# Kernel optimization log

Hardware: AMD Instinct MI355X
Metric: run time of the kernel (lower is better)

Reference implementation:

```python
import jax, jax.numpy as jnp
import numpy as np

N_LAYERS = 4
H = 16
LOOKBACK = 128  # cross_window
EPS = 1e-6
ROPE_BASE = 10000.0
NEG = jnp.float32(-1e30)


def rmsnorm(x, w):
    return x * jax.lax.rsqrt(jnp.mean(x * x, axis=-1, keepdims=True) + EPS) * w


def rope_cache(L, hd):
    inv = 1.0 / (ROPE_BASE ** (jnp.arange(0, hd, 2, dtype=jnp.float32) / hd))
    t = jnp.arange(L, dtype=jnp.float32)
    f = t[:, None] * inv[None, :]            # [L, hd/2]
    emb = jnp.concatenate([f, f], axis=-1)   # [L, hd]
    return jnp.cos(emb), jnp.sin(emb)


def apply_rope(x, cos, sin):
    # x: [B,H,L,d]; rotate-half convention
    d = x.shape[-1]
    x1, x2 = x[..., : d // 2], x[..., d // 2:]
    rot = jnp.concatenate([-x2, x1], axis=-1)
    return x * cos + rot * sin


def split_heads(x, n_heads):
    B, L, D = x.shape
    return x.reshape(B, L, n_heads, D // n_heads).transpose(0, 2, 1, 3)


def merge_heads(x):
    B, h, L, d = x.shape
    return x.transpose(0, 2, 1, 3).reshape(B, L, h * d)


def sdpa(q, k, v, bias):
    scale = q.shape[-1] ** -0.5
    s = jnp.einsum('bhqd,bhkd->bhqk', q, k) * scale + bias
    p = jax.nn.softmax(s, axis=-1)
    return jnp.einsum('bhqk,bhkd->bhqd', p, v)


def forward(x, memory, seg_ids, Wqkv, bqkv, Wo, bo, Wq_c, Wkv_c, Wo_c, Wg, Wu, Wd, n1, n2, n3, nf):
    B, L, D = x.shape
    S = memory.shape[1]
    hd = D // H
    cos, sin = rope_cache(L, hd)

    # causal additive mask [1,1,L,L]
    i = jnp.arange(L)
    causal_bias = jnp.where(i[None, :] <= i[:, None], 0.0, NEG)[None, None]

    # segment-causal sliding-window cross mask [B,1,L,S]:
    # token t may attend memory j with seg_id[t]-LOOKBACK < j <= seg_id[t]
    j = jnp.arange(S)
    allowed = (j[None, None, :] <= seg_ids[:, :, None]) & (j[None, None, :] > seg_ids[:, :, None] - LOOKBACK)
    cross_bias = jnp.where(allowed, 0.0, NEG)[:, None]  # [B,1,L,S]

    for l in range(N_LAYERS):
        # --- causal self-attn with RoPE ---
        h = rmsnorm(x, n1[l])
        qkv = h @ Wqkv[l].T + bqkv[l]                      # [B,L,3D]
        q, k, v = jnp.split(qkv, 3, axis=-1)
        q = apply_rope(split_heads(q, H), cos, sin)
        k = apply_rope(split_heads(k, H), cos, sin)
        v = split_heads(v, H)
        o = merge_heads(sdpa(q, k, v, causal_bias)) @ Wo[l].T + bo[l]
        x = x + o

        # --- segment-causal sliding-window cross-attn ---
        h2 = rmsnorm(x, n2[l])
        qc = split_heads(h2 @ Wq_c[l].T, H)
        kv = memory @ Wkv_c[l].T                           # [B,S,2D]
        kc, vc = jnp.split(kv, 2, axis=-1)
        kc, vc = split_heads(kc, H), split_heads(vc, H)
        oc = merge_heads(sdpa(qc, kc, vc, cross_bias)) @ Wo_c[l].T
        x = x + oc

        # --- SwiGLU FFN ---
        h3 = rmsnorm(x, n3[l])
        x = x + (jax.nn.silu(h3 @ Wg[l].T) * (h3 @ Wu[l].T)) @ Wd[l].T

    return rmsnorm(x, nf)


def setup_inputs() -> dict:
    key = jax.random.key(0)
    ks = jax.random.split(key, 16)
    B, L, S, D, F = 2, 2048, 256, 1024, 4096
    w = 0.02
    inp = {
        'x': jax.random.normal(ks[0], (B, L, D), jnp.float32),
        'memory': jax.random.normal(ks[1], (B, S, D), jnp.float32),
        'seg_ids': jnp.sort(jax.random.randint(ks[2], (B, L), 0, S), axis=-1),
        'Wqkv': jax.random.normal(ks[3], (N_LAYERS, 3 * D, D), jnp.float32) * w,
        'bqkv': jnp.zeros((N_LAYERS, 3 * D), jnp.float32),
        'Wo': jax.random.normal(ks[4], (N_LAYERS, D, D), jnp.float32) * w,
        'bo': jnp.zeros((N_LAYERS, D), jnp.float32),
        'Wq_c': jax.random.normal(ks[5], (N_LAYERS, D, D), jnp.float32) * w,
        'Wkv_c': jax.random.normal(ks[6], (N_LAYERS, 2 * D, D), jnp.float32) * w,
        'Wo_c': jax.random.normal(ks[7], (N_LAYERS, D, D), jnp.float32) * w,
        'Wg': jax.random.normal(ks[8], (N_LAYERS, F, D), jnp.float32) * w,
        'Wu': jax.random.normal(ks[9], (N_LAYERS, F, D), jnp.float32) * w,
        'Wd': jax.random.normal(ks[10], (N_LAYERS, D, F), jnp.float32) * w,
        'n1': jnp.ones((N_LAYERS, D), jnp.float32),
        'n2': jnp.ones((N_LAYERS, D), jnp.float32),
        'n3': jnp.ones((N_LAYERS, D), jnp.float32),
        'nf': jnp.ones((D,), jnp.float32),
    }
    return inp


def reference(x, memory, seg_ids, Wqkv, bqkv, Wo, bo, Wq_c, Wkv_c, Wo_c, Wg, Wu, Wd, n1, n2, n3, nf):
    return forward(x, memory, seg_ids, Wqkv, bqkv, Wo, bo, Wq_c, Wkv_c, Wo_c, Wg, Wu, Wd, n1, n2, n3, nf)
```

## Files before the change

kernel.cpp:

```cpp
#include <hip/hip_runtime.h>
#include <hip/hip_bf16.h>
#include <math.h>

#define N_LAYERS 4
#define NHEADS 16
#define LOOKBACK 128

typedef unsigned short ushort_t;
typedef __attribute__((ext_vector_type(8))) short short8;
typedef __attribute__((ext_vector_type(4))) float f32x4;

__device__ __forceinline__ ushort_t f2bf(float f) {
    union { float f; unsigned int u; } v; v.f = f;
    unsigned int r = (v.u + 0x7FFFu + ((v.u >> 16) & 1u)) >> 16;
    return (ushort_t)r;
}
__device__ __forceinline__ float bf2f(ushort_t s) {
    union { unsigned int u; float f; } v; v.u = ((unsigned int)s) << 16;
    return v.f;
}

__device__ __forceinline__ float blk_sum(float v, volatile float* red) {
#pragma unroll
    for (int o = 32; o > 0; o >>= 1) v += __shfl_down(v, o, 64);
    if ((threadIdx.x & 63) == 0) red[threadIdx.x >> 6] = v;
    __syncthreads();
    float r = red[0] + red[1] + red[2] + red[3];
    __syncthreads();
    return r;
}

__global__ __launch_bounds__(256) void f2b_k(const float* __restrict__ in,
                                             ushort_t* __restrict__ out, int n4) {
    int i = blockIdx.x * 256 + threadIdx.x;
    if (i >= n4) return;
    float4 v = *(const float4*)(in + (size_t)i * 4);
    ushort_t* o = out + (size_t)i * 4;
    o[0] = f2bf(v.x); o[1] = f2bf(v.y); o[2] = f2bf(v.z); o[3] = f2bf(v.w);
}

__global__ __launch_bounds__(256) void rmsnorm_bf(const float* __restrict__ x,
                                                  const float* __restrict__ w,
                                                  ushort_t* __restrict__ out, int D) {
    __shared__ float red[4];
    size_t row = blockIdx.x;
    const float* xr = x + row * D;
    float ss = 0.f;
    for (int i = threadIdx.x; i < D; i += 256) { float v = xr[i]; ss += v * v; }
    float tot = blk_sum(ss, red);
    float r = rsqrtf(tot / (float)D + 1e-6f);
    ushort_t* o = out + row * D;
    for (int i = threadIdx.x; i < D; i += 256) o[i] = f2bf(xr[i] * r * w[i]);
}

__global__ __launch_bounds__(256) void rmsnorm_k(const float* __restrict__ x,
                                                 const float* __restrict__ w,
                                                 float* __restrict__ out, int D) {
    __shared__ float red[4];
    size_t row = blockIdx.x;
    const float* xr = x + row * D;
    float ss = 0.f;
    for (int i = threadIdx.x; i < D; i += 256) { float v = xr[i]; ss += v * v; }
    float tot = blk_sum(ss, red);
    float r = rsqrtf(tot / (float)D + 1e-6f);
    float* o = out + row * D;
    for (int i = threadIdx.x; i < D; i += 256) o[i] = xr[i] * r * w[i];
}

#define GBM 128
#define GBN 128
#define GBK 32

#define STAGE_GEMM(kk, buf) do {                                               \
    const ushort_t* Ag_ = A + (size_t)(bm + srow) * K + (kk) + c4 * 8;         \
    const ushort_t* Bg_ = Bw + (size_t)(bn + srow) * K + (kk) + c4 * 8;        \
    __builtin_amdgcn_global_load_lds(                                          \
        (const __attribute__((address_space(1))) void*)Ag_,                    \
        (__attribute__((address_space(3))) void*)&As[buf][wave * 16 * GBK],    \
        16, 0, 0);                                                             \
    __builtin_amdgcn_global_load_lds(                                          \
        (const __attribute__((address_space(1))) void*)(Ag_ + (size_t)64 * K), \
        (__attribute__((address_space(3))) void*)&As[buf][(64 + wave * 16) * GBK], \
        16, 0, 0);                                                             \
    __builtin_amdgcn_global_load_lds(                                          \
        (const __attribute__((address_space(1))) void*)Bg_,                    \
        (__attribute__((address_space(3))) void*)&Bs[buf][wave * 16 * GBK],    \
        16, 0, 0);                                                             \
    __builtin_amdgcn_global_load_lds(                                          \
        (const __attribute__((address_space(1))) void*)(Bg_ + (size_t)64 * K), \
        (__attribute__((address_space(3))) void*)&Bs[buf][(64 + wave * 16) * GBK], \
        16, 0, 0);                                                             \
} while (0)

__global__ __launch_bounds__(256) void gemm_bf16(
    const ushort_t* __restrict__ A, const ushort_t* __restrict__ Bw,
    void* __restrict__ Cout, const float* __restrict__ bias,
    const float* __restrict__ resid, const ushort_t* __restrict__ gate,
    int M, int N, int K, int out_bf16) {
    __shared__ ushort_t As[2][GBM * GBK];
    __shared__ ushort_t Bs[2][GBN * GBK];
    int tid = threadIdx.x;
    int wave = tid >> 6, lane = tid & 63;
    int nwg = gridDim.x * gridDim.y;
    int wg  = blockIdx.y * gridDim.x + blockIdx.x;
    int qq = nwg >> 3, rr = nwg & 7;
    int xcd = wg & 7, loc = wg >> 3;
    int swz = (xcd < rr ? xcd * (qq + 1) : rr * (qq + 1) + (xcd - rr) * qq) + loc;
    int bm = (swz / gridDim.x) * GBM, bn = (swz % gridDim.x) * GBN;
    int wm = (wave & 1) * 64, wn = (wave >> 1) * 64;
    int r4 = lane >> 2, c4 = lane & 3;
    int r = lane & 15, q = lane >> 4;

    f32x4 acc[4][4];
#pragma unroll
    for (int i = 0; i < 4; ++i)
#pragma unroll
        for (int j = 0; j < 4; ++j) acc[i][j] = (f32x4){0.f, 0.f, 0.f, 0.f};

    int srow = wave * 16 + r4;
    int nt = K / GBK;
    STAGE_GEMM(0, 0);
    for (int t = 0; t < nt; ++t) {
        int cur = t & 1;
        if (t + 1 < nt) {
            STAGE_GEMM((t + 1) * GBK, cur ^ 1);
            asm volatile("s_waitcnt vmcnt(4)" ::: "memory");
        } else {
            asm volatile("s_waitcnt vmcnt(0)" ::: "memory");
        }
        __builtin_amdgcn_s_barrier();
        __builtin_amdgcn_sched_barrier(0);
        short8 af[4], bfr[4];
#pragma unroll
        for (int i = 0; i < 4; ++i)
            af[i] = *(const short8*)&As[cur][(wm + 16 * i + r) * GBK + q * 8];
#pragma unroll
        for (int j = 0; j < 4; ++j)
            bfr[j] = *(const short8*)&Bs[cur][(wn + 16 * j + r) * GBK + q * 8];
#pragma unroll
        for (int i = 0; i < 4; ++i)
#pragma unroll
            for (int j = 0; j < 4; ++j)
                acc[i][j] = __builtin_amdgcn_mfma_f32_16x16x32_bf16(
                    af[i], bfr[j], acc[i][j], 0, 0, 0);
        __builtin_amdgcn_s_barrier();
        __builtin_amdgcn_sched_barrier(0);
    }
#pragma unroll
    for (int i = 0; i < 4; ++i) {
#pragma unroll
        for (int j = 0; j < 4; ++j) {
            size_t n = (size_t)(bn + wn + 16 * j + r);
            float bn_v = bias ? bias[n] : 0.f;
#pragma unroll
            for (int t = 0; t < 4; ++t) {
                size_t m = (size_t)(bm + wm + 16 * i + q * 4 + t);
                size_t idx = m * N + n;
                float x = acc[i][j][t] + bn_v;
                if (gate) { float g = bf2f(gate[idx]); x *= g / (1.0f + __expf(-g)); }
                if (resid) x += resid[idx];
                if (out_bf16) ((ushort_t*)Cout)[idx] = f2bf(x);
                else ((float*)Cout)[idx] = x;
            }
        }
    }
}

__global__ void rope_k(ushort_t* __restrict__ qkv, int L, int total) {
    int idx = blockIdx.x * 256 + threadIdx.x;
    if (idx >= total) return;
    int d = idx & 31;
    int h = (idx >> 5) & 15;
    int bl = idx >> 9;
    int l = bl % L;
    float inv = exp2f(-(float)d * (13.2877123795f / 32.0f));
    float f = (float)l * inv;
    float s, c;
    sincosf(f, &s, &c);
    ushort_t* base = qkv + (size_t)bl * 3072 + h * 64 + d;
    float x1 = bf2f(base[0]), x2 = bf2f(base[32]);
    base[0]  = f2bf((x1 * c - x2 * s) * 0.125f);
    base[32] = f2bf((x2 * c + x1 * s) * 0.125f);
    ushort_t* kb = base + 1024;
    x1 = bf2f(kb[0]); x2 = bf2f(kb[32]);
    kb[0]  = f2bf(x1 * c - x2 * s);
    kb[32] = f2bf(x2 * c + x1 * s);
}

#define QB 128

__global__ __launch_bounds__(256) void self_attn_flash(
    const ushort_t* __restrict__ qkv, ushort_t* __restrict__ out, int L) {
    int lin = blockIdx.x + gridDim.x * (blockIdx.y + gridDim.y * blockIdx.z);
    int xcd = lin & 7, slot = lin >> 3;
    int qt = slot & 15;
    int grp = xcd + 8 * (slot >> 4);
    int h = grp & 15, b = grp >> 4;
    int q0 = qt * QB;

    __shared__ ushort_t Qs[QB * 72];
    __shared__ ushort_t Ks[2][64 * 72];
    __shared__ ushort_t VT[2][64 * 64];
    __shared__ ushort_t Ps[QB * 64];

    int tid = threadIdx.x;
    int wave = tid >> 6, lane = tid & 63;
    int g = lane >> 4, r = lane & 15;
    int lr2 = tid >> 1, lc2 = tid & 1;
    int lr = tid >> 2, lc = tid & 3;

    {
        const ushort_t* src = qkv + ((size_t)b * L + q0 + lr2) * 3072 + h * 64 + lc2 * 32;
        ushort_t* dst = &Qs[lr2 * 72 + lc2 * 32];
        *(short8*)(dst)      = *(const short8*)(src);
        *(short8*)(dst + 8)  = *(const short8*)(src + 8);
        *(short8*)(dst + 16) = *(const short8*)(src + 16);
        *(short8*)(dst + 24) = *(const short8*)(src + 24);
    }
    __syncthreads();
    short8 aq[2][2];
#pragma unroll
    for (int s = 0; s < 2; ++s)
#pragma unroll
        for (int c = 0; c < 2; ++c)
            aq[s][c] = *(const short8*)&Qs[(wave * 32 + s * 16 + r) * 72 + c * 32 + g * 8];

    const ushort_t* kvbase = qkv + ((size_t)b * L + lr) * 3072 + 1024 + h * 64 + lc * 16;
    short8 kreg0 = *(const short8*)(kvbase);
    short8 kreg1 = *(const short8*)(kvbase + 8);
    short8 vreg0 = *(const short8*)(kvbase + 1024);
    short8 vreg1 = *(const short8*)(kvbase + 1032);

    float m[2][4], lsum[2][4];
    f32x4 acc[2][4];
#pragma unroll
    for (int s = 0; s < 2; ++s)
#pragma unroll
        for (int t = 0; t < 4; ++t) { m[s][t] = -1e30f; lsum[s][t] = 0.f; }
#pragma unroll
    for (int s = 0; s < 2; ++s)
#pragma unroll
        for (int j = 0; j < 4; ++j) acc[s][j] = (f32x4){0.f, 0.f, 0.f, 0.f};

    int ktmax = 2 * qt + 1;
    for (int kt = 0; kt <= ktmax; ++kt) {
        int cb = kt & 1;
        ushort_t* Kc = &Ks[cb][0];
        ushort_t* Vc = &VT[cb][0];
        *(short8*)&Kc[lr * 72 + lc * 16]     = kreg0;
        *(short8*)&Kc[lr * 72 + lc * 16 + 8] = kreg1;
#pragma unroll
        for (int i = 0; i < 8; ++i) {
            int row0 = lc * 16 + i;
            int f0 = (row0 & 7) ^ ((row0 >> 4) & 3);
            Vc[row0 * 64 + (((lr >> 3) ^ f0) << 3) + (lr & 7)] = (ushort_t)vreg0[i];
            int row1 = row0 + 8;
            int f1 = (row1 & 7) ^ ((row1 >> 4) & 3);
            Vc[row1 * 64 + (((lr >> 3) ^ f1) << 3) + (lr & 7)] = (ushort_t)vreg1[i];
        }
        asm volatile("s_waitcnt lgkmcnt(0)" ::: "memory");
        __builtin_amdgcn_s_barrier();
        __builtin_amdgcn_sched_barrier(0);
        if (kt < ktmax) {
            const ushort_t* p = kvbase + (size_t)(kt + 1) * 64 * 3072;
            kreg0 = *(const short8*)(p);
            kreg1 = *(const short8*)(p + 8);
            vreg0 = *(const short8*)(p + 1024);
            vreg1 = *(const short8*)(p + 1032);
        }

        int k0 = kt * 64;
        f32x4 s2[2][4];
#pragma unroll
        for (int s = 0; s < 2; ++s)
#pragma unroll
            for (int j = 0; j < 4; ++j) s2[s][j] = (f32x4){0.f, 0.f, 0.f, 0.f};
        __builtin_amdgcn_s_setprio(1);
#pragma unroll
        for (int j = 0; j < 4; ++j)
#pragma unroll
            for (int c = 0; c < 2; ++c) {
                short8 bk = *(const short8*)&Kc[(16 * j + r) * 72 + c * 32 + g * 8];
                s2[0][j] = __builtin_amdgcn_mfma_f32_16x16x32_bf16(aq[0][c], bk, s2[0][j], 0, 0, 0);
                s2[1][j] = __builtin_amdgcn_mfma_f32_16x16x32_bf16(aq[1][c], bk, s2[1][j], 0, 0, 0);
            }
        __builtin_amdgcn_s_setprio(0);

        if (kt >= ktmax - 1) {
#pragma unroll
            for (int s = 0; s < 2; ++s)
#pragma unroll
                for (int j = 0; j < 4; ++j) {
                    int k = k0 + 16 * j + r;
#pragma unroll
                    for (int t = 0; t < 4; ++t)
                        if (k > q0 + wave * 32 + s * 16 + 4 * g + t) s2[s][j][t] = -1e30f;
                }
        }

        float al[2][4];
#pragma unroll
        for (int s = 0; s < 2; ++s)
#pragma unroll
            for (int t = 0; t < 4; ++t) {
                float rm = fmaxf(fmaxf(s2[s][0][t], s2[s][1][t]), fmaxf(s2[s][2][t], s2[s][3][t]));
#pragma unroll
                for (int o = 8; o > 0; o >>= 1) rm = fmaxf(rm, __shfl_xor(rm, o, 16));
                float mn = fmaxf(m[s][t], rm);
                al[s][t] = __expf(m[s][t] - mn);
                m[s][t] = mn;
                float rs = 0.f;
#pragma unroll
                for (int j = 0; j < 4; ++j) {
                    float p = __expf(s2[s][j][t] - mn);
                    s2[s][j][t] = p;
                    rs += p;
                }
#pragma unroll
                for (int o = 8; o > 0; o >>= 1) rs += __shfl_xor(rs, o, 16);
                lsum[s][t] = lsum[s][t] * al[s][t] + rs;
            }

#pragma unroll
        for (int s = 0; s < 2; ++s)
#pragma unroll
            for (int j = 0; j < 4; ++j)
#pragma unroll
                for (int t = 0; t < 4; ++t) {
                    int row = wave * 32 + s * 16 + 4 * g + t;
                    int f = (row >> 1) & 7;
                    Ps[row * 64 + (((2 * j + (r >> 3)) ^ f) << 3) + (r & 7)] = f2bf(s2[s][j][t]);
                }
        short8 ap[2][2];
#pragma unroll
        for (int s = 0; s < 2; ++s) {
            int row = wave * 32 + s * 16 + r;
            int f = (row >> 1) & 7;
#pragma unroll
            for (int c = 0; c < 2; ++c)
                ap[s][c] = *(const short8*)&Ps[row * 64 + (((4 * c + g) ^ f) << 3)];
        }

#pragma unroll
        for (int s = 0; s < 2; ++s)
#pragma unroll
            for (int j = 0; j < 4; ++j)
#pragma unroll
                for (int t = 0; t < 4; ++t) acc[s][j][t] *= al[s][t];
        __builtin_amdgcn_s_setprio(1);
#pragma unroll
        for (int j = 0; j < 4; ++j)
#pragma unroll
            for (int c = 0; c < 2; ++c) {
                int row = 16 * j + r;
                int ch = (4 * c + g) ^ (r & 7) ^ j;
                short8 bv = *(const short8*)&Vc[row * 64 + (ch << 3)];
                acc[0][j] = __builtin_amdgcn_mfma_f32_16x16x32_bf16(ap[0][c], bv, acc[0][j], 0, 0, 0);
                acc[1][j] = __builtin_amdgcn_mfma_f32_16x16x32_bf16(ap[1][c], bv, acc[1][j], 0, 0, 0);
            }
        __builtin_amdgcn_s_setprio(0);
    }

#pragma unroll
    for (int s = 0; s < 2; ++s)
#pragma unroll
        for (int t = 0; t < 4; ++t) {
            float invl = 1.0f / lsum[s][t];
            size_t orow = ((size_t)b * L + q0 + wave * 32 + s * 16 + 4 * g + t) * 1024 + h * 64;
#pragma unroll
            for (int j = 0; j < 4; ++j)
                out[orow + 16 * j + r] = f2bf(acc[s][j][t] * invl);
        }
}

#define AP 72

__global__ __launch_bounds__(256) void cross_attn_mfma(
    const ushort_t* __restrict__ qc, const ushort_t* __restrict__ kvc,
    const int* __restrict__ seg_ids, ushort_t* __restrict__ out, int L, int S) {
    int qt = blockIdx.x, h = blockIdx.y, b = blockIdx.z;
    int q0 = qt * 64;
    __shared__ ushort_t Qs[64 * AP];
    __shared__ ushort_t Ks[64 * AP];
    __shared__ ushort_t VT[64 * AP];
    __shared__ ushort_t Ps[64 * AP];
    __shared__ int segs[64];
    __shared__ int bounds[2];
    int tid = threadIdx.x;
    int wave = tid >> 6, lane = tid & 63;
    int g = lane >> 4, r = lane & 15;
    int lr = tid >> 2, lc = tid & 3;

    {
        const ushort_t* src = qc + ((size_t)b * L + q0 + lr) * 1024 + h * 64 + lc * 16;
        *(short8*)&Qs[lr * AP + lc * 16]     = *(const short8*)(src);
        *(short8*)&Qs[lr * AP + lc * 16 + 8] = *(const short8*)(src + 8);
    }
    if (tid < 64) segs[tid] = seg_ids[(size_t)b * L + q0 + tid];
    __syncthreads();
    if (wave == 0) {
        int v = segs[lane];
        int mn = v, mx = v;
#pragma unroll
        for (int o = 32; o > 0; o >>= 1) {
            mn = min(mn, __shfl_down(mn, o, 64));
            mx = max(mx, __shfl_down(mx, o, 64));
        }
        if (lane == 0) { bounds[0] = mn; bounds[1] = mx; }
    }
    int seg_t[4];
#pragma unroll
    for (int t = 0; t < 4; ++t) seg_t[t] = segs[wave * 16 + 4 * g + t];
    short8 aq[2];
#pragma unroll
    for (int c = 0; c < 2; ++c)
        aq[c] = *(const short8*)&Qs[(wave * 16 + r) * AP + c * 32 + g * 8];
    __syncthreads();
    int lo = bounds[0] - (LOOKBACK - 1); if (lo < 0) lo = 0;
    int t_lo = lo >> 6;
    int t_hi = bounds[1] >> 6;

    float m[4]    = {-1e30f, -1e30f, -1e30f, -1e30f};
    float lsum[4] = {0.f, 0.f, 0.f, 0.f};
    f32x4 acc[4];
#pragma unroll
    for (int j = 0; j < 4; ++j) acc[j] = (f32x4){0.f, 0.f, 0.f, 0.f};

    for (int kt = t_lo; kt <= t_hi; ++kt) {
        int k0 = kt * 64;
        __syncthreads();
        {
            const ushort_t* ksrc = kvc + ((size_t)b * S + k0 + lr) * 2048 + h * 64 + lc * 16;
            short8 k0v = *(const short8*)(ksrc);
            short8 k1v = *(const short8*)(ksrc + 8);
            *(short8*)&Ks[lr * AP + lc * 16]     = k0v;
            *(short8*)&Ks[lr * AP + lc * 16 + 8] = k1v;
            const ushort_t* vsrc = ksrc + 1024;
            short8 v0v = *(const short8*)(vsrc);
            short8 v1v = *(const short8*)(vsrc + 8);
#pragma unroll
            for (int i = 0; i < 8; ++i) {
                VT[(lc * 16 + i) * AP + lr]     = (ushort_t)v0v[i];
                VT[(lc * 16 + 8 + i) * AP + lr] = (ushort_t)v1v[i];
            }
        }
        __syncthreads();

        f32x4 s[4];
#pragma unroll
        for (int j = 0; j < 4; ++j) s[j] = (f32x4){0.f, 0.f, 0.f, 0.f};
#pragma unroll
        for (int j = 0; j < 4; ++j)
#pragma unroll
            for (int c = 0; c < 2; ++c) {
                short8 bk = *(const short8*)&Ks[(16 * j + r) * AP + c * 32 + g * 8];
                s[j] = __builtin_amdgcn_mfma_f32_16x16x32_bf16(aq[c], bk, s[j], 0, 0, 0);
            }

#pragma unroll
        for (int j = 0; j < 4; ++j) {
            int k = k0 + 16 * j + r;
#pragma unroll
            for (int t = 0; t < 4; ++t) {
                float v = s[j][t] * 0.125f;
                if (k > seg_t[t] || k <= seg_t[t] - LOOKBACK) v = -1e30f;
                s[j][t] = v;
            }
        }

        float al[4];
#pragma unroll
        for (int t = 0; t < 4; ++t) {
            float rm = fmaxf(fmaxf(s[0][t], s[1][t]), fmaxf(s[2][t], s[3][t]));
#pragma unroll
            for (int o = 8; o > 0; o >>= 1) rm = fmaxf(rm, __shfl_xor(rm, o, 16));
            float mn = fmaxf(m[t], rm);
            al[t] = __expf(m[t] - mn);
            m[t] = mn;
            float rs = 0.f;
#pragma unroll
            for (int j = 0; j < 4; ++j) {
                float p = __expf(s[j][t] - mn);
                s[j][t] = p;
                rs += p;
            }
#pragma unroll
            for (int o = 8; o > 0; o >>= 1) rs += __shfl_xor(rs, o, 16);
            lsum[t] = lsum[t] * al[t] + rs;
        }

        ushort_t* pw = &Ps[wave * 16 * AP];
#pragma unroll
        for (int j = 0; j < 4; ++j)
#pragma unroll
            for (int t = 0; t < 4; ++t)
                pw[(4 * g + t) * AP + 16 * j + r] = f2bf(s[j][t]);
        short8 ap[2];
#pragma unroll
        for (int c = 0; c < 2; ++c)
            ap[c] = *(const short8*)&pw[r * AP + c * 32 + g * 8];

#pragma unroll
        for (int j = 0; j < 4; ++j) {
#pragma unroll
            for (int t = 0; t < 4; ++t) acc[j][t] *= al[t];
#pragma unroll
            for (int c = 0; c < 2; ++c) {
                short8 bv = *(const short8*)&VT[(16 * j + r) * AP + c * 32 + g * 8];
                acc[j] = __builtin_amdgcn_mfma_f32_16x16x32_bf16(ap[c], bv, acc[j], 0, 0, 0);
            }
        }
    }

#pragma unroll
    for (int t = 0; t < 4; ++t) {
        float invl = 1.0f / lsum[t];
        size_t orow = ((size_t)b * L + q0 + wave * 16 + 4 * g + t) * 1024 + h * 64;
#pragma unroll
        for (int j = 0; j < 4; ++j)
            out[orow + 16 * j + r] = f2bf(acc[j][t] * invl);
    }
}

extern "C" void kernel_launch(void* const* d_in, const int* in_sizes, int n_in,
                              void* d_out, int out_size, void* d_ws, size_t ws_size,
                              hipStream_t stream) {
    const int B = 2, L = 2048, S = 256, D = 1024, F = 4096;
    const int BL = B * L;
    const float* x_in   = (const float*)d_in[0];
    const float* memory = (const float*)d_in[1];
    const int*   seg    = (const int*)d_in[2];
    const float* Wqkv = (const float*)d_in[3];
    const float* bqkv = (const float*)d_in[4];
    const float* Wo   = (const float*)d_in[5];
    const float* bo   = (const float*)d_in[6];
    const float* Wq_c = (const float*)d_in[7];
    const float* Wkv_c= (const float*)d_in[8];
    const float* Wo_c = (const float*)d_in[9];
    const float* Wg   = (const float*)d_in[10];
    const float* Wu   = (const float*)d_in[11];
    const float* Wd   = (const float*)d_in[12];
    const float* n1   = (const float*)d_in[13];
    const float* n2   = (const float*)d_in[14];
    const float* n3   = (const float*)d_in[15];
    const float* nf   = (const float*)d_in[16];

    char* ws = (char*)d_ws;
    size_t off = 0;
    float* X     = (float*)(ws + off); off += (size_t)BL * D * 4;
    float* QKV   = (float*)(ws + off); off += (size_t)BL * 3 * D * 4;
    float* KVC   = (float*)(ws + off); off += (size_t)B * S * 2 * D * 4;
    ushort_t* Hn  = (ushort_t*)(ws + off); off += (size_t)BL * D * 2;
    ushort_t* Abf = (ushort_t*)(ws + off); off += (size_t)BL * D * 2;
    ushort_t* Mb  = (ushort_t*)(ws + off); off += (size_t)B * S * D * 2;
    ushort_t* Wb  = (ushort_t*)(ws + off); off += (size_t)F * D * 2;
    ushort_t* QKVb = (ushort_t*)QKV;
    ushort_t* Qcb  = (ushort_t*)QKV;
    ushort_t* KVCb = (ushort_t*)KVC;
    ushort_t* Gg = (ushort_t*)QKV;

    hipMemcpyAsync(X, x_in, (size_t)BL * D * sizeof(float), hipMemcpyDeviceToDevice, stream);

    dim3 blk(256);
    f2b_k<<<(B * S * D / 4 + 255) / 256, blk, 0, stream>>>(memory, Mb, B * S * D / 4);

    for (int l = 0; l < N_LAYERS; ++l) {
        rmsnorm_bf<<<BL, blk, 0, stream>>>(X, n1 + (size_t)l * D, Hn, D);
        f2b_k<<<(3 * D * D / 4 + 255) / 256, blk, 0, stream>>>(
            Wqkv + (size_t)l * 3 * D * D, Wb, 3 * D * D / 4);
        gemm_bf16<<<dim3(3 * D / GBN, BL / GBM), blk, 0, stream>>>(
            Hn, Wb, QKVb, bqkv + (size_t)l * 3 * D, nullptr, nullptr, BL, 3 * D, D, 1);
        int total = BL * NHEADS * 32;
        rope_k<<<(total + 255) / 256, blk, 0, stream>>>(QKVb, L, total);
        self_attn_flash<<<dim3(L / QB, NHEADS, B), blk, 0, stream>>>(QKVb, Abf, L);
        f2b_k<<<(D * D / 4 + 255) / 256, blk, 0, stream>>>(
            Wo + (size_t)l * D * D, Wb, D * D / 4);
        gemm_bf16<<<dim3(D / GBN, BL / GBM), blk, 0, stream>>>(
            Abf, Wb, X, bo + (size_t)l * D, X, nullptr, BL, D, D, 0);
        rmsnorm_bf<<<BL, blk, 0, stream>>>(X, n2 + (size_t)l * D, Hn, D);
        f2b_k<<<(D * D / 4 + 255) / 256, blk, 0, stream>>>(
            Wq_c + (size_t)l * D * D, Wb, D * D / 4);
        gemm_bf16<<<dim3(D / GBN, BL / GBM), blk, 0, stream>>>(
            Hn, Wb, Qcb, nullptr, nullptr, nullptr, BL, D, D, 1);
        f2b_k<<<(2 * D * D / 4 + 255) / 256, blk, 0, stream>>>(
            Wkv_c + (size_t)l * 2 * D * D, Wb, 2 * D * D / 4);
        gemm_bf16<<<dim3(2 * D / GBN, B * S / GBM), blk, 0, stream>>>(
            Mb, Wb, KVCb, nullptr, nullptr, nullptr, B * S, 2 * D, D, 1);
        cross_attn_mfma<<<dim3(L / 64, NHEADS, B), blk, 0, stream>>>(
            Qcb, KVCb, seg, Abf, L, S);
        f2b_k<<<(D * D / 4 + 255) / 256, blk, 0, stream>>>(
            Wo_c + (size_t)l * D * D, Wb, D * D / 4);
        gemm_bf16<<<dim3(D / GBN, BL / GBM), blk, 0, stream>>>(
            Abf, Wb, X, nullptr, X, nullptr, BL, D, D, 0);
        rmsnorm_bf<<<BL, blk, 0, stream>>>(X, n3 + (size_t)l * D, Hn, D);
        f2b_k<<<(F * D / 4 + 255) / 256, blk, 0, stream>>>(
            Wg + (size_t)l * F * D, Wb, F * D / 4);
        gemm_bf16<<<dim3(F / GBN, BL / GBM), blk, 0, stream>>>(
            Hn, Wb, Gg, nullptr, nullptr, nullptr, BL, F, D, 1);
        f2b_k<<<(F * D / 4 + 255) / 256, blk, 0, stream>>>(
            Wu + (size_t)l * F * D, Wb, F * D / 4);
        gemm_bf16<<<dim3(F / GBN, BL / GBM), blk, 0, stream>>>(
            Hn, Wb, Gg, nullptr, nullptr, Gg, BL, F, D, 1);
        f2b_k<<<(D * F / 4 + 255) / 256, blk, 0, stream>>>(
            Wd + (size_t)l * D * F, Wb, D * F / 4);
        gemm_bf16<<<dim3(D / GBN, BL / GBM), blk, 0, stream>>>(
            Gg, Wb, X, nullptr, X, nullptr, BL, D, F, 0);
    }
    rmsnorm_k<<<BL, blk, 0, stream>>>(X, nf, (float*)d_out, D);
}
```

Baseline: 2.718 ms.

## Balance causal self-attention by pairing complementary 64-row query tiles per block

Each block now handles two 64-row query tiles, pair and 31-pair, one after the other, so every block does the same amount of causal work. Before, each block took one 128-row tile, and cost grew with the tile index. Q fragments are loaded straight from global memory into registers instead of staging through shared memory. A lazy rescale skips the exp/accumulator rescale unless the new row max exceeds the running max by more than 8, and row sums are reduced across lanes only once at the end. The risk is less MFMA reuse per K/V tile, since each wave now covers 16 rows instead of 32, so K/V shared-memory traffic per query doubles.

```diff
diff --git a/kernel.cpp b/kernel.cpp
--- a/kernel.cpp
+++ b/kernel.cpp
@@ -187,190 +187,169 @@
     kb[32] = f2bf(x2 * c + x1 * s);
 }
 
-#define QB 128
-
 __global__ __launch_bounds__(256) void self_attn_flash(
     const ushort_t* __restrict__ qkv, ushort_t* __restrict__ out, int L) {
     int lin = blockIdx.x + gridDim.x * (blockIdx.y + gridDim.y * blockIdx.z);
     int xcd = lin & 7, slot = lin >> 3;
-    int qt = slot & 15;
+    int pair = slot & 15;
     int grp = xcd + 8 * (slot >> 4);
     int h = grp & 15, b = grp >> 4;
-    int q0 = qt * QB;
-
-    __shared__ ushort_t Qs[QB * 72];
+
     __shared__ ushort_t Ks[2][64 * 72];
     __shared__ ushort_t VT[2][64 * 64];
-    __shared__ ushort_t Ps[QB * 64];
+    __shared__ ushort_t Ps[64 * 64];
 
     int tid = threadIdx.x;
     int wave = tid >> 6, lane = tid & 63;
     int g = lane >> 4, r = lane & 15;
-    int lr2 = tid >> 1, lc2 = tid & 1;
     int lr = tid >> 2, lc = tid & 3;
 
-    {
-        const ushort_t* src = qkv + ((size_t)b * L + q0 + lr2) * 3072 + h * 64 + lc2 * 32;
-        ushort_t* dst = &Qs[lr2 * 72 + lc2 * 32];
-        *(short8*)(dst)      = *(const short8*)(src);
-        *(short8*)(dst + 8)  = *(const short8*)(src + 8);
-        *(short8*)(dst + 16) = *(const short8*)(src + 16);
-        *(short8*)(dst + 24) = *(const short8*)(src + 24);
-    }
-    __syncthreads();
-    short8 aq[2][2];
-#pragma unroll
-    for (int s = 0; s < 2; ++s)
-#pragma unroll
-        for (int c = 0; c < 2; ++c)
-            aq[s][c] = *(const short8*)&Qs[(wave * 32 + s * 16 + r) * 72 + c * 32 + g * 8];
-
     const ushort_t* kvbase = qkv + ((size_t)b * L + lr) * 3072 + 1024 + h * 64 + lc * 16;
-    short8 kreg0 = *(const short8*)(kvbase);
-    short8 kreg1 = *(const short8*)(kvbase + 8);
-    short8 vreg0 = *(const short8*)(kvbase + 1024);
-    short8 vreg1 = *(const short8*)(kvbase + 1032);
-
-    float m[2][4], lsum[2][4];
-    f32x4 acc[2][4];
-#pragma unroll
-    for (int s = 0; s < 2; ++s)
-#pragma unroll
-        for (int t = 0; t < 4; ++t) { m[s][t] = -1e30f; lsum[s][t] = 0.f; }
-#pragma unroll
-    for (int s = 0; s < 2; ++s)
-#pragma unroll
-        for (int j = 0; j < 4; ++j) acc[s][j] = (f32x4){0.f, 0.f, 0.f, 0.f};
-
-    int ktmax = 2 * qt + 1;
-    for (int kt = 0; kt <= ktmax; ++kt) {
-        int cb = kt & 1;
-        ushort_t* Kc = &Ks[cb][0];
-        ushort_t* Vc = &VT[cb][0];
-        *(short8*)&Kc[lr * 72 + lc * 16]     = kreg0;
-        *(short8*)&Kc[lr * 72 + lc * 16 + 8] = kreg1;
-#pragma unroll
-        for (int i = 0; i < 8; ++i) {
-            int row0 = lc * 16 + i;
-            int f0 = (row0 & 7) ^ ((row0 >> 4) & 3);
-            Vc[row0 * 64 + (((lr >> 3) ^ f0) << 3) + (lr & 7)] = (ushort_t)vreg0[i];
-            int row1 = row0 + 8;
-            int f1 = (row1 & 7) ^ ((row1 >> 4) & 3);
-            Vc[row1 * 64 + (((lr >> 3) ^ f1) << 3) + (lr & 7)] = (ushort_t)vreg1[i];
-        }
-        asm volatile("s_waitcnt lgkmcnt(0)" ::: "memory");
-        __builtin_amdgcn_s_barrier();
-        __builtin_amdgcn_sched_barrier(0);
-        if (kt < ktmax) {
-            const ushort_t* p = kvbase + (size_t)(kt + 1) * 64 * 3072;
-            kreg0 = *(const short8*)(p);
-            kreg1 = *(const short8*)(p + 8);
-            vreg0 = *(const short8*)(p + 1024);
-            vreg1 = *(const short8*)(p + 1032);
-        }
-
-        int k0 = kt * 64;
-        f32x4 s2[2][4];
-#pragma unroll
-        for (int s = 0; s < 2; ++s)
-#pragma unroll
-            for (int j = 0; j < 4; ++j) s2[s][j] = (f32x4){0.f, 0.f, 0.f, 0.f};
-        __builtin_amdgcn_s_setprio(1);
-#pragma unroll
-        for (int j = 0; j < 4; ++j)
-#pragma unroll
-            for (int c = 0; c < 2; ++c) {
-                short8 bk = *(const short8*)&Kc[(16 * j + r) * 72 + c * 32 + g * 8];
-                s2[0][j] = __builtin_amdgcn_mfma_f32_16x16x32_bf16(aq[0][c], bk, s2[0][j], 0, 0, 0);
-                s2[1][j] = __builtin_amdgcn_mfma_f32_16x16x32_bf16(aq[1][c], bk, s2[1][j], 0, 0, 0);
-            }
-        __builtin_amdgcn_s_setprio(0);
-
-        if (kt >= ktmax - 1) {
-#pragma unroll
-            for (int s = 0; s < 2; ++s)
+
+    for (int ph = 0; ph < 2; ++ph) {
+        int qt = ph ? 31 - pair : pair;
+        int q0 = qt * 64;
+
+        const ushort_t* qrow = qkv + ((size_t)b * L + q0 + wave * 16 + r) * 3072 + h * 64 + g * 8;
+        short8 aq0 = *(const short8*)(qrow);
+        short8 aq1 = *(const short8*)(qrow + 32);
+
+        short8 kreg0 = *(const short8*)(kvbase);
+        short8 kreg1 = *(const short8*)(kvbase + 8);
+        short8 vreg0 = *(const short8*)(kvbase + 1024);
+        short8 vreg1 = *(const short8*)(kvbase + 1032);
+
+        if (ph) {
+            __builtin_amdgcn_s_barrier();
+            __builtin_amdgcn_sched_barrier(0);
+        }
+
+        float m[4]  = {-1e30f, -1e30f, -1e30f, -1e30f};
+        float lp[4] = {0.f, 0.f, 0.f, 0.f};
+        f32x4 acc[4];
+#pragma unroll
+        for (int j = 0; j < 4; ++j) acc[j] = (f32x4){0.f, 0.f, 0.f, 0.f};
+
+        for (int kt = 0; kt <= qt; ++kt) {
+            int cb = kt & 1;
+            ushort_t* Kc = &Ks[cb][0];
+            ushort_t* Vc = &VT[cb][0];
+            *(short8*)&Kc[lr * 72 + lc * 16]     = kreg0;
+            *(short8*)&Kc[lr * 72 + lc * 16 + 8] = kreg1;
+#pragma unroll
+            for (int i = 0; i < 8; ++i) {
+                int row0 = lc * 16 + i;
+                int f0 = (row0 & 7) ^ ((row0 >> 4) & 3);
+                Vc[row0 * 64 + (((lr >> 3) ^ f0) << 3) + (lr & 7)] = (ushort_t)vreg0[i];
+                int row1 = row0 + 8;
+                int f1 = (row1 & 7) ^ ((row1 >> 4) & 3);
+                Vc[row1 * 64 + (((lr >> 3) ^ f1) << 3) + (lr & 7)] = (ushort_t)vreg1[i];
+            }
+            asm volatile("s_waitcnt lgkmcnt(0)" ::: "memory");
+            __builtin_amdgcn_s_barrier();
+            __builtin_amdgcn_sched_barrier(0);
+            if (kt < qt) {
+                const ushort_t* p = kvbase + (size_t)(kt + 1) * 64 * 3072;
+                kreg0 = *(const short8*)(p);
+                kreg1 = *(const short8*)(p + 8);
+                vreg0 = *(const short8*)(p + 1024);
+                vreg1 = *(const short8*)(p + 1032);
+            }
+
+            f32x4 s[4];
+#pragma unroll
+            for (int j = 0; j < 4; ++j) s[j] = (f32x4){0.f, 0.f, 0.f, 0.f};
+            __builtin_amdgcn_s_setprio(1);
+#pragma unroll
+            for (int j = 0; j < 4; ++j) {
+                short8 bk0 = *(const short8*)&Kc[(16 * j + r) * 72 + g * 8];
+                s[j] = __builtin_amdgcn_mfma_f32_16x16x32_bf16(aq0, bk0, s[j], 0, 0, 0);
+                short8 bk1 = *(const short8*)&Kc[(16 * j + r) * 72 + 32 + g * 8];
+                s[j] = __builtin_amdgcn_mfma_f32_16x16x32_bf16(aq1, bk1, s[j], 0, 0, 0);
+            }
+            __builtin_amdgcn_s_setprio(0);
+
+            if (kt == qt) {
+#pragma unroll
+                for (int j = 0; j < 4; ++j)
+#pragma unroll
+                    for (int t = 0; t < 4; ++t)
+                        if (16 * j + r > wave * 16 + 4 * g + t) s[j][t] = -1e30f;
+            }
+
+            float rm[4];
+            bool need = false;
+#pragma unroll
+            for (int t = 0; t < 4; ++t) {
+                float x = fmaxf(fmaxf(s[0][t], s[1][t]), fmaxf(s[2][t], s[3][t]));
+#pragma unroll
+                for (int o = 8; o > 0; o >>= 1) x = fmaxf(x, __shfl_xor(x, o, 16));
+                rm[t] = x;
+                need = need || (x > m[t] + 8.f);
+            }
+            if (__any((int)need)) {
+#pragma unroll
+                for (int t = 0; t < 4; ++t) {
+                    float mn = fmaxf(m[t], rm[t]);
+                    float al = __expf(m[t] - mn);
+                    m[t] = mn;
+                    lp[t] *= al;
+#pragma unroll
+                    for (int j = 0; j < 4; ++j) acc[j][t] *= al;
+                }
+            }
+#pragma unroll
+            for (int t = 0; t < 4; ++t) {
 #pragma unroll
                 for (int j = 0; j < 4; ++j) {
-                    int k = k0 + 16 * j + r;
-#pragma unroll
-                    for (int t = 0; t < 4; ++t)
-                        if (k > q0 + wave * 32 + s * 16 + 4 * g + t) s2[s][j][t] = -1e30f;
+                    float p = __expf(s[j][t] - m[t]);
+                    s[j][t] = p;
+                    lp[t] += p;
                 }
-        }
-
-        float al[2][4];
-#pragma unroll
-        for (int s = 0; s < 2; ++s)
-#pragma unroll
-            for (int t = 0; t < 4; ++t) {
-                float rm = fmaxf(fmaxf(s2[s][0][t], s2[s][1][t]), fmaxf(s2[s][2][t], s2[s][3][t]));
-#pragma unroll
-                for (int o = 8; o > 0; o >>= 1) rm = fmaxf(rm, __shfl_xor(rm, o, 16));
-                float mn = fmaxf(m[s][t], rm);
-                al[s][t] = __expf(m[s][t] - mn);
-                m[s][t] = mn;
-                float rs = 0.f;
-#pragma unroll
-                for (int j = 0; j < 4; ++j) {
-                    float p = __expf(s2[s][j][t] - mn);
-                    s2[s][j][t] = p;
-                    rs += p;
+            }
+
+#pragma unroll
+            for (int j = 0; j < 4; ++j)
+#pragma unroll
+                for (int t = 0; t < 4; ++t) {
+                    int row = wave * 16 + 4 * g + t;
+                    int f = (row >> 1) & 7;
+                    Ps[row * 64 + (((2 * j + (r >> 3)) ^ f) << 3) + (r & 7)] = f2bf(s[j][t]);
                 }
-#pragma unroll
-                for (int o = 8; o > 0; o >>= 1) rs += __shfl_xor(rs, o, 16);
-                lsum[s][t] = lsum[s][t] * al[s][t] + rs;
-            }
-
-#pragma unroll
-        for (int s = 0; s < 2; ++s)
+            short8 ap0, ap1;
+            {
+                int row = wave * 16 + r;
+                int f = (row >> 1) & 7;
+                ap0 = *(const short8*)&Ps[row * 64 + ((g ^ f) << 3)];
+                ap1 = *(const short8*)&Ps[row * 64 + (((4 + g) ^ f) << 3)];
+            }
+
+            __builtin_amdgcn_s_setprio(1);
+#pragma unroll
+            for (int j = 0; j < 4; ++j) {
+                int rowv = 16 * j + r;
+                int ch0 = g ^ (r & 7) ^ j;
+                short8 bv0 = *(const short8*)&Vc[rowv * 64 + (ch0 << 3)];
+                acc[j] = __builtin_amdgcn_mfma_f32_16x16x32_bf16(ap0, bv0, acc[j], 0, 0, 0);
+                int ch1 = (4 + g) ^ (r & 7) ^ j;
+                short8 bv1 = *(const short8*)&Vc[rowv * 64 + (ch1 << 3)];
+                acc[j] = __builtin_amdgcn_mfma_f32_16x16x32_bf16(ap1, bv1, acc[j], 0, 0, 0);
+            }
+            __builtin_amdgcn_s_setprio(0);
+        }
+
+#pragma unroll
+        for (int t = 0; t < 4; ++t) {
+            float tot = lp[t];
+#pragma unroll
+            for (int o = 8; o > 0; o >>= 1) tot += __shfl_xor(tot, o, 16);
+            float invl = 1.0f / tot;
+            size_t orow = ((size_t)b * L + q0 + wave * 16 + 4 * g + t) * 1024 + h * 64;
 #pragma unroll
             for (int j = 0; j < 4; ++j)
-#pragma unroll
-                for (int t = 0; t < 4; ++t) {
-                    int row = wave * 32 + s * 16 + 4 * g + t;
-                    int f = (row >> 1) & 7;
-                    Ps[row * 64 + (((2 * j + (r >> 3)) ^ f) << 3) + (r & 7)] = f2bf(s2[s][j][t]);
-                }
-        short8 ap[2][2];
-#pragma unroll
-        for (int s = 0; s < 2; ++s) {
-            int row = wave * 32 + s * 16 + r;
-            int f = (row >> 1) & 7;
-#pragma unroll
-            for (int c = 0; c < 2; ++c)
-                ap[s][c] = *(const short8*)&Ps[row * 64 + (((4 * c + g) ^ f) << 3)];
-        }
-
-#pragma unroll
-        for (int s = 0; s < 2; ++s)
-#pragma unroll
-            for (int j = 0; j < 4; ++j)
-#pragma unroll
-                for (int t = 0; t < 4; ++t) acc[s][j][t] *= al[s][t];
-        __builtin_amdgcn_s_setprio(1);
-#pragma unroll
-        for (int j = 0; j < 4; ++j)
-#pragma unroll
-            for (int c = 0; c < 2; ++c) {
-                int row = 16 * j + r;
-                int ch = (4 * c + g) ^ (r & 7) ^ j;
-                short8 bv = *(const short8*)&Vc[row * 64 + (ch << 3)];
-                acc[0][j] = __builtin_amdgcn_mfma_f32_16x16x32_bf16(ap[0][c], bv, acc[0][j], 0, 0, 0);
-                acc[1][j] = __builtin_amdgcn_mfma_f32_16x16x32_bf16(ap[1][c], bv, acc[1][j], 0, 0, 0);
-            }
-        __builtin_amdgcn_s_setprio(0);
-    }
-
-#pragma unroll
-    for (int s = 0; s < 2; ++s)
-#pragma unroll
-        for (int t = 0; t < 4; ++t) {
-            float invl = 1.0f / lsum[s][t];
-            size_t orow = ((size_t)b * L + q0 + wave * 32 + s * 16 + 4 * g + t) * 1024 + h * 64;
-#pragma unroll
-            for (int j = 0; j < 4; ++j)
-                out[orow + 16 * j + r] = f2bf(acc[s][j][t] * invl);
-        }
+                out[orow + 16 * j + r] = f2bf(acc[j][t] * invl);
+        }
+    }
 }
 
 #define AP 72
@@ -572,7 +551,7 @@
             Hn, Wb, QKVb, bqkv + (size_t)l * 3 * D, nullptr, nullptr, BL, 3 * D, D, 1);
         int total = BL * NHEADS * 32;
         rope_k<<<(total + 255) / 256, blk, 0, stream>>>(QKVb, L, total);
-        self_attn_flash<<<dim3(L / QB, NHEADS, B), blk, 0, stream>>>(QKVb, Abf, L);
+        self_attn_flash<<<dim3(L / 128, NHEADS, B), blk, 0, stream>>>(QKVb, Abf, L);
         f2b_k<<<(D * D / 4 + 255) / 256, blk, 0, stream>>>(
             Wo + (size_t)l * D * D, Wb, D * D / 4);
         gemm_bf16<<<dim3(D / GBN, BL / GBM), blk, 0, stream>>>(
```

New measurement: 2.533 ms. -6.8%, faster.
